# Optimization experiments

Measured on AMD Instinct MI355X. Metric: run time of the kernel, lower is better.

The kernel has to match this reference:

```python
import jax, jax.numpy as jnp
import numpy as np

N = 50000      # nodes
E = 1_600_000  # edges
F_IN = 128; HID = 128; LAT = 64; OUT = 128; GEN = 2


def gcn_conv(x, src, dst, norm, W, b, n_nodes):
    """PyG GCNConv with self-loops already appended to (src, dst) and
    symmetric normalization `norm` precomputed per edge."""
    h = x @ W                                    # [N, out]
    msg = h[src] * norm[:, None]                 # [E+N, out] gather + scale
    out = jax.ops.segment_sum(msg, dst, num_segments=n_nodes)
    return out + b


def _self_loop_norm(edge_index, n_nodes):
    loops = jnp.arange(n_nodes, dtype=edge_index.dtype)
    src = jnp.concatenate([edge_index[0], loops])
    dst = jnp.concatenate([edge_index[1], loops])
    deg = jnp.zeros((n_nodes,), jnp.float32).at[dst].add(1.0)
    dinv = jnp.where(deg > 0, deg ** -0.5, 0.0)
    norm = dinv[src] * dinv[dst]
    return src, dst, norm


def setup_inputs() -> dict:
    key = jax.random.key(0)
    ks = jax.random.split(key, 12)
    p = lambda k, s: jax.random.normal(k, s, jnp.float32) * 0.05
    return {
        "x": jax.random.normal(ks[0], (N, F_IN), jnp.float32),
        "edge_index": jax.random.randint(ks[1], (2, E), 0, N, jnp.int32),
        "eps": jax.random.normal(ks[2], (N, LAT), jnp.float32),
        "u": jax.random.uniform(ks[3], (N, GEN), jnp.float32),
        "W1": p(ks[4], (F_IN, HID)), "b1": jnp.zeros((HID,), jnp.float32),
        "W_mu": p(ks[5], (HID, LAT)), "b_mu": jnp.zeros((LAT,), jnp.float32),
        "W_ls": p(ks[6], (HID, LAT)), "b_ls": jnp.zeros((LAT,), jnp.float32),
        "W_dx": p(ks[7], (LAT, OUT)), "b_dx": jnp.zeros((OUT,), jnp.float32),
        "W_g": p(ks[8], (LAT, GEN)), "b_g": jnp.zeros((GEN,), jnp.float32),
        "W_lc": p(ks[9], (LAT, 1)), "b_lc": jnp.zeros((1,), jnp.float32),
    }


def reference(x, edge_index, eps, u, W1, b1, W_mu, b_mu, W_ls, b_ls,
              W_dx, b_dx, W_g, b_g, W_lc, b_lc):
    n = x.shape[0]
    src, dst, norm = _self_loop_norm(edge_index, n)

    # Encoder: GCN -> relu -> (mu, logvar)
    h = jax.nn.relu(gcn_conv(x, src, dst, norm, W1, b1, n))
    mu = gcn_conv(h, src, dst, norm, W_mu, b_mu, n)
    logvar = gcn_conv(h, src, dst, norm, W_ls, b_ls, n)

    # reparameterize: z = eps * exp(0.5*logvar) + mu
    z = eps * jnp.exp(0.5 * logvar) + mu

    # decoders / classifiers
    recon_x = gcn_conv(z, src, dst, norm, W_dx, b_dx, n)
    logits_gender = gcn_conv(z, src, dst, norm, W_g, b_g, n)
    logits_label = z @ W_lc + b_lc

    # Gumbel-softmax (hard, straight-through), temperature=1.0
    g = -jnp.log(-jnp.log(u + 1e-20) + 1e-20)
    y_soft = jax.nn.softmax(logits_gender + g, axis=-1)
    y_hard = jax.nn.one_hot(jnp.argmax(y_soft, axis=-1), GEN, dtype=y_soft.dtype)
    gender = jax.lax.stop_gradient(y_hard - y_soft) + y_soft

    return (recon_x, gender, logits_label, mu, logvar, z)
```

## Files before the change

### kernel.cpp

```cpp
#include <hip/hip_runtime.h>
#include <hip/hip_fp16.h>
#include <cstddef>


constexpr int R = 200;
constexpr int NBUCK = 250;
constexpr int NBLK = 250;
constexpr int SLABCAP = 12288;

__global__ __launch_bounds__(256) void hist_kernel(
    const int* __restrict__ dst, int* __restrict__ gh, int e, int chunk) {
  __shared__ int h[NBUCK];
  for (int t = threadIdx.x; t < NBUCK; t += 256) h[t] = 0;
  __syncthreads();
  int beg = blockIdx.x * chunk;
  int fin = min(e, beg + chunk);
  for (int i = beg + threadIdx.x; i < fin; i += 256)
    atomicAdd(&h[dst[i] / R], 1);
  __syncthreads();
  for (int t = threadIdx.x; t < NBUCK; t += 256)
    gh[t * NBLK + blockIdx.x] = h[t];
}

__global__ void scan_p1(const int* __restrict__ in, int* __restrict__ part, int n) {
  __shared__ int s[256];
  int i = blockIdx.x * 256 + threadIdx.x;
  s[threadIdx.x] = (i < n) ? in[i] : 0;
  __syncthreads();
  for (int off = 128; off > 0; off >>= 1) {
    if (threadIdx.x < off) s[threadIdx.x] += s[threadIdx.x + off];
    __syncthreads();
  }
  if (threadIdx.x == 0) part[blockIdx.x] = s[0];
}

__global__ void scan_p2(int* __restrict__ part, int nb, int* __restrict__ total_out) {
  __shared__ int s[256];
  int v = (threadIdx.x < nb) ? part[threadIdx.x] : 0;
  s[threadIdx.x] = v;
  __syncthreads();
  for (int off = 1; off < 256; off <<= 1) {
    int t = (threadIdx.x >= off) ? s[threadIdx.x - off] : 0;
    __syncthreads();
    s[threadIdx.x] += t;
    __syncthreads();
  }
  if (threadIdx.x < nb) part[threadIdx.x] = s[threadIdx.x] - v;
  if (threadIdx.x == nb - 1) *total_out = s[threadIdx.x];
}

__global__ void scan_p3(int* io, const int* __restrict__ part, int n) {
  __shared__ int s[256];
  int i = blockIdx.x * 256 + threadIdx.x;
  int v = (i < n) ? io[i] : 0;
  s[threadIdx.x] = v;
  __syncthreads();
  for (int off = 1; off < 256; off <<= 1) {
    int t = (threadIdx.x >= off) ? s[threadIdx.x - off] : 0;
    __syncthreads();
    s[threadIdx.x] += t;
    __syncthreads();
  }
  int excl = s[threadIdx.x] - v + part[blockIdx.x];
  if (i < n) io[i] = excl;
}

__global__ __launch_bounds__(256) void scatter_kernel(
    const int* __restrict__ src, const int* __restrict__ dst,
    const int* __restrict__ ghs, int* __restrict__ binned, int e, int chunk) {
  __shared__ int cur[NBUCK];
  for (int t = threadIdx.x; t < NBUCK; t += 256)
    cur[t] = ghs[t * NBLK + blockIdx.x];
  __syncthreads();
  int beg = blockIdx.x * chunk;
  int fin = min(e, beg + chunk);
  for (int i = beg + threadIdx.x; i < fin; i += 256) {
    int d = dst[i];
    int b = d / R;
    int p = atomicAdd(&cur[b], 1);
    binned[p] = ((d - b * R) << 16) | src[i];
  }
}

__global__ __launch_bounds__(256) void final_kernel(
    const int* __restrict__ binned, const int* __restrict__ ghs,
    int* __restrict__ rowptr, int* __restrict__ csr,
    float* __restrict__ dinv, int n, int e) {
  __shared__ int sdeg[R];
  __shared__ int sscan[256];
  __shared__ int scur[R];
  __shared__ int slab[SLABCAP];
  const int b = blockIdx.x;
  const int tid = threadIdx.x;
  const int base = ghs[b * NBLK];
  const int end = (b < NBUCK - 1) ? ghs[(b + 1) * NBLK] : e;
  const int cnt = end - base;

  if (tid < R) sdeg[tid] = 0;
  __syncthreads();
  for (int k = base + tid; k < end; k += 256)
    atomicAdd(&sdeg[binned[k] >> 16], 1);
  __syncthreads();

  int dv = (tid < R) ? sdeg[tid] : 0;
  sscan[tid] = dv;
  __syncthreads();
  for (int off = 1; off < 256; off <<= 1) {
    int t = (tid >= off) ? sscan[tid - off] : 0;
    __syncthreads();
    sscan[tid] += t;
    __syncthreads();
  }
  int excl = sscan[tid] - dv;
  int node = b * R + tid;
  if (tid < R && node < n) {
    rowptr[node] = base + excl;
    dinv[node] = 1.0f / sqrtf((float)dv + 1.0f);
    scur[tid] = excl;
  }
  __syncthreads();

  const bool fits = (cnt <= SLABCAP);
  for (int k = base + tid; k < end; k += 256) {
    int rec = binned[k];
    int p = atomicAdd(&scur[rec >> 16], 1);
    int s = rec & 0xFFFF;
    if (fits) slab[p] = s;
    else csr[base + p] = s;
  }
  __syncthreads();
  if (fits)
    for (int k = tid; k < cnt; k += 256) csr[base + k] = slab[k];
}

template <int K, int M, int KT, int RPT, bool BIAS, bool RELU, bool HALF_OUT>
__global__ __launch_bounds__(256, 4) void gemm_kernel(
    const float* __restrict__ A, const float* __restrict__ W,
    const float* __restrict__ bias, float* __restrict__ C,
    __half* __restrict__ Ch, const float* __restrict__ dinv, int n) {
  constexpr int CG = M / 4;
  constexpr int RS = 256 / CG;
  constexpr int RPB = RS * RPT;
  __shared__ float sW[KT * M];
  const int cg = threadIdx.x % CG;
  const int rs = threadIdx.x / CG;
  const int row0 = blockIdx.x * RPB + rs * RPT;

  const float* Arow[RPT];
#pragma unroll
  for (int rr = 0; rr < RPT; ++rr) {
    int row = row0 + rr;
    if (row > n - 1) row = n - 1;
    Arow[rr] = A + (size_t)row * K;
  }

  float4 acc[RPT];
#pragma unroll
  for (int rr = 0; rr < RPT; ++rr) acc[rr] = float4{0.f, 0.f, 0.f, 0.f};

  for (int kt = 0; kt < K; kt += KT) {
    if (kt) __syncthreads();
    for (int i = threadIdx.x * 4; i < KT * M; i += 1024)
      *reinterpret_cast<float4*>(&sW[i]) =
          *reinterpret_cast<const float4*>(&W[kt * M + i]);
    __syncthreads();
#pragma unroll 4
    for (int k4 = 0; k4 < KT; k4 += 4) {
      float4 a[RPT];
#pragma unroll
      for (int rr = 0; rr < RPT; ++rr)
        a[rr] = *reinterpret_cast<const float4*>(Arow[rr] + kt + k4);
#pragma unroll
      for (int j = 0; j < 4; ++j) {
        float4 w = *reinterpret_cast<const float4*>(&sW[(k4 + j) * M + cg * 4]);
#pragma unroll
        for (int rr = 0; rr < RPT; ++rr) {
          float av = reinterpret_cast<const float*>(&a[rr])[j];
          acc[rr].x += av * w.x;
          acc[rr].y += av * w.y;
          acc[rr].z += av * w.z;
          acc[rr].w += av * w.w;
        }
      }
    }
  }

  float4 bv = float4{0.f, 0.f, 0.f, 0.f};
  if (BIAS) bv = *reinterpret_cast<const float4*>(&bias[cg * 4]);
#pragma unroll
  for (int rr = 0; rr < RPT; ++rr) {
    int row = row0 + rr;
    if (row < n) {
      float4 o = acc[rr];
      if (BIAS) { o.x += bv.x; o.y += bv.y; o.z += bv.z; o.w += bv.w; }
      if (RELU) {
        o.x = fmaxf(o.x, 0.f); o.y = fmaxf(o.y, 0.f);
        o.z = fmaxf(o.z, 0.f); o.w = fmaxf(o.w, 0.f);
      }
      if (HALF_OUT) {
        float di = dinv[row];
        __half2* dst = reinterpret_cast<__half2*>(Ch + (size_t)row * M + cg * 4);
        dst[0] = __floats2half2_rn(di * o.x, di * o.y);
        dst[1] = __floats2half2_rn(di * o.z, di * o.w);
      } else {
        *reinterpret_cast<float4*>(&C[(size_t)row * M + cg * 4]) = o;
      }
    }
  }
}

template <int VAR, bool BIAS, bool RELU, bool HALF_OUT>
__global__ __launch_bounds__(256) void spmm128_kernel(
    const __half* __restrict__ Xs, void* __restrict__ Yout,
    const int* __restrict__ rowptr, const int* __restrict__ csr,
    const float* __restrict__ dinv, const float* __restrict__ bias, int n) {
  int wid = (blockIdx.x * blockDim.x + threadIdx.x) >> 6;
  int lane = threadIdx.x & 63;
  if (wid >= n) return;
  int beg = rowptr[wid];
  int end = rowptr[wid + 1];
  constexpr int U = (VAR == 0) ? 8 : 16;
  constexpr int NA = 8;
  float a0[NA], a1[NA];
#pragma unroll
  for (int uu = 0; uu < NA; ++uu) { a0[uu] = 0.f; a1[uu] = 0.f; }

  for (int base = beg; base < end; base += 64) {
    int m = end - base;
    if (m > 64) m = 64;
    int idx = (lane < m) ? csr[base + lane] : 0;
    int j = 0;
    for (; j + U <= m; j += U) {
      const __half2* rows[U];
#pragma unroll
      for (int uu = 0; uu < U; ++uu)
        rows[uu] = reinterpret_cast<const __half2*>(
            Xs + (size_t)__shfl(idx, j + uu, 64) * 128);
      __half2 v[U];
#pragma unroll
      for (int uu = 0; uu < U; ++uu) v[uu] = rows[uu][lane];
#pragma unroll
      for (int uu = 0; uu < U; ++uu) {
        float2 f = __half22float2(v[uu]);
        a0[uu & (NA - 1)] += f.x;
        a1[uu & (NA - 1)] += f.y;
      }
    }
    for (; j < m; ++j) {
      const __half2* row = reinterpret_cast<const __half2*>(
          Xs + (size_t)__shfl(idx, j, 64) * 128);
      float2 f = __half22float2(row[lane]);
      a0[0] += f.x;
      a1[0] += f.y;
    }
  }

  float t0 = 0.f, t1 = 0.f;
#pragma unroll
  for (int uu = 0; uu < NA; ++uu) { t0 += a0[uu]; t1 += a1[uu]; }

  float2 sf = __half22float2(
      reinterpret_cast<const __half2*>(Xs + (size_t)wid * 128)[lane]);
  t0 += sf.x;
  t1 += sf.y;

  float di = dinv[wid];
  float r0 = di * t0;
  float r1 = di * t1;
  if (BIAS) { r0 += bias[lane * 2]; r1 += bias[lane * 2 + 1]; }
  if (RELU) { r0 = fmaxf(r0, 0.f); r1 = fmaxf(r1, 0.f); }

  if (HALF_OUT) {
    reinterpret_cast<__half2*>((__half*)Yout + (size_t)wid * 128)[lane] =
        __floats2half2_rn(di * r0, di * r1);
  } else {
    float2 o = {r0, r1};
    reinterpret_cast<float2*>((float*)Yout + (size_t)wid * 128)[lane] = o;
  }
}

__global__ __launch_bounds__(256, 4) void mlz_kernel(
    const float* __restrict__ hagg,
    const float* __restrict__ Wmu, const float* __restrict__ bmu,
    const float* __restrict__ Wls, const float* __restrict__ bls,
    const float* __restrict__ eps, const float* __restrict__ dinv,
    const float* __restrict__ Wg, const float* __restrict__ Wlc,
    const float* __restrict__ blc,
    float* __restrict__ out_mu, float* __restrict__ out_lv,
    float* __restrict__ out_z, unsigned int* __restrict__ zh8,
    float2* __restrict__ zgs, float* __restrict__ out_label, int n) {
  constexpr int K = 128, M = 64, KT = 64, RPT = 4;
  constexpr int CG = M / 4;
  constexpr int RS = 256 / CG;
  constexpr int RPB = RS * RPT;
  __shared__ float sWm[KT * M];
  __shared__ float sWl[KT * M];
  const int cg = threadIdx.x % CG;
  const int rs = threadIdx.x / CG;
  const int row0 = blockIdx.x * RPB + rs * RPT;

  const float* Arow[RPT];
#pragma unroll
  for (int rr = 0; rr < RPT; ++rr) {
    int row = row0 + rr;
    if (row > n - 1) row = n - 1;
    Arow[rr] = hagg + (size_t)row * K;
  }

  float4 am[RPT], al[RPT];
#pragma unroll
  for (int rr = 0; rr < RPT; ++rr) {
    am[rr] = float4{0.f, 0.f, 0.f, 0.f};
    al[rr] = float4{0.f, 0.f, 0.f, 0.f};
  }

  for (int kt = 0; kt < K; kt += KT) {
    if (kt) __syncthreads();
    for (int i = threadIdx.x * 4; i < KT * M; i += 1024) {
      *reinterpret_cast<float4*>(&sWm[i]) =
          *reinterpret_cast<const float4*>(&Wmu[kt * M + i]);
      *reinterpret_cast<float4*>(&sWl[i]) =
          *reinterpret_cast<const float4*>(&Wls[kt * M + i]);
    }
    __syncthreads();
#pragma unroll 2
    for (int k4 = 0; k4 < KT; k4 += 4) {
      float4 a[RPT];
#pragma unroll
      for (int rr = 0; rr < RPT; ++rr)
        a[rr] = *reinterpret_cast<const float4*>(Arow[rr] + kt + k4);
#pragma unroll
      for (int j = 0; j < 4; ++j) {
        float4 wm = *reinterpret_cast<const float4*>(&sWm[(k4 + j) * M + cg * 4]);
        float4 wl = *reinterpret_cast<const float4*>(&sWl[(k4 + j) * M + cg * 4]);
#pragma unroll
        for (int rr = 0; rr < RPT; ++rr) {
          float av = reinterpret_cast<const float*>(&a[rr])[j];
          am[rr].x += av * wm.x; am[rr].y += av * wm.y;
          am[rr].z += av * wm.z; am[rr].w += av * wm.w;
          al[rr].x += av * wl.x; al[rr].y += av * wl.y;
          al[rr].z += av * wl.z; al[rr].w += av * wl.w;
        }
      }
    }
  }

  float4 bm = *reinterpret_cast<const float4*>(&bmu[cg * 4]);
  float4 bl = *reinterpret_cast<const float4*>(&bls[cg * 4]);
  float wg0[4], wg1[4], wlcv[4];
#pragma unroll
  for (int cc = 0; cc < 4; ++cc) {
    int c = cg * 4 + cc;
    wg0[cc] = Wg[c * 2 + 0];
    wg1[cc] = Wg[c * 2 + 1];
    wlcv[cc] = Wlc[c];
  }
  float blc0 = blc[0];

#pragma unroll
  for (int rr = 0; rr < RPT; ++rr) {
    int row = row0 + rr;
    if (row < n) {
      float4 mu4 = {am[rr].x + bm.x, am[rr].y + bm.y,
                    am[rr].z + bm.z, am[rr].w + bm.w};
      float4 lv4 = {al[rr].x + bl.x, al[rr].y + bl.y,
                    al[rr].z + bl.z, al[rr].w + bl.w};
      float4 e4 = *reinterpret_cast<const float4*>(&eps[(size_t)row * 64 + cg * 4]);
      float4 z4 = {e4.x * expf(0.5f * lv4.x) + mu4.x,
                   e4.y * expf(0.5f * lv4.y) + mu4.y,
                   e4.z * expf(0.5f * lv4.z) + mu4.z,
                   e4.w * expf(0.5f * lv4.w) + mu4.w};
      *reinterpret_cast<float4*>(&out_mu[(size_t)row * 64 + cg * 4]) = mu4;
      *reinterpret_cast<float4*>(&out_lv[(size_t)row * 64 + cg * 4]) = lv4;
      *reinterpret_cast<float4*>(&out_z[(size_t)row * 64 + cg * 4]) = z4;
      float di = dinv[row];
      int pw = __builtin_amdgcn_cvt_pk_fp8_f32(di * z4.x, di * z4.y, 0, false);
      pw = __builtin_amdgcn_cvt_pk_fp8_f32(di * z4.z, di * z4.w, pw, true);
      zh8[(size_t)row * 16 + cg] = (unsigned int)pw;
      float pg0 = z4.x * wg0[0] + z4.y * wg0[1] + z4.z * wg0[2] + z4.w * wg0[3];
      float pg1 = z4.x * wg1[0] + z4.y * wg1[1] + z4.z * wg1[2] + z4.w * wg1[3];
      float pl  = z4.x * wlcv[0] + z4.y * wlcv[1] + z4.z * wlcv[2] + z4.w * wlcv[3];
#pragma unroll
      for (int off = 1; off < 16; off <<= 1) {
        pg0 += __shfl_xor(pg0, off, 64);
        pg1 += __shfl_xor(pg1, off, 64);
        pl  += __shfl_xor(pl, off, 64);
      }
      if (cg == 0) {
        zgs[row] = float2{di * pg0, di * pg1};
        out_label[row] = pl + blc0;
      }
    }
  }
}

__device__ __forceinline__ void fp8x4acc(unsigned d, float* a) {
#if defined(__has_builtin) && __has_builtin(__builtin_amdgcn_cvt_pk_f32_fp8)
  typedef float f32x2 __attribute__((ext_vector_type(2)));
  f32x2 lo = __builtin_amdgcn_cvt_pk_f32_fp8((int)d, false);
  f32x2 hi = __builtin_amdgcn_cvt_pk_f32_fp8((int)d, true);
  a[0] += lo.x; a[1] += lo.y; a[2] += hi.x; a[3] += hi.y;
#else
  a[0] += __builtin_amdgcn_cvt_f32_fp8((int)d, 0);
  a[1] += __builtin_amdgcn_cvt_f32_fp8((int)d, 1);
  a[2] += __builtin_amdgcn_cvt_f32_fp8((int)d, 2);
  a[3] += __builtin_amdgcn_cvt_f32_fp8((int)d, 3);
#endif
}

__global__ __launch_bounds__(256) void spmm_zg_kernel(
    const unsigned char* __restrict__ zh8, const float2* __restrict__ zgs,
    float* __restrict__ zagg, const int* __restrict__ rowptr,
    const int* __restrict__ csr, const float* __restrict__ dinv,
    const float* __restrict__ bg, const float* __restrict__ u,
    float* __restrict__ out_gender, int n) {
  int wid = (blockIdx.x * blockDim.x + threadIdx.x) >> 6;
  int lane = threadIdx.x & 63;
  if (wid >= n) return;
  int beg = rowptr[wid];
  int end = rowptr[wid + 1];
  const int g = lane >> 4;
  const int c = lane & 15;
  const int coff = c * 4;

  float accA[4], accB[4];
#pragma unroll
  for (int f = 0; f < 4; ++f) { accA[f] = 0.f; accB[f] = 0.f; }
  float ga0 = 0.f, ga1 = 0.f;

  for (int base = beg; base < end; base += 64) {
    int m = end - base;
    if (m > 64) m = 64;
    int idx = 0;
    if (lane < m) {
      idx = csr[base + lane];
      float2 gz = zgs[idx];
      ga0 += gz.x;
      ga1 += gz.y;
    }
    int j = 0;
    for (; j + 8 <= m; j += 8) {
      int i0 = __shfl(idx, j + g, 64);
      int i1 = __shfl(idx, j + 4 + g, 64);
      unsigned d0 = *reinterpret_cast<const unsigned*>(
          zh8 + (size_t)(unsigned)i0 * 64 + coff);
      unsigned d1 = *reinterpret_cast<const unsigned*>(
          zh8 + (size_t)(unsigned)i1 * 64 + coff);
      fp8x4acc(d0, accA);
      fp8x4acc(d1, accB);
    }
    if (j < m) {
      int e0 = j + g;
      int e1 = j + 4 + g;
      int i0 = __shfl(idx, min(e0, m - 1), 64);
      int i1 = __shfl(idx, min(e1, m - 1), 64);
      unsigned d0 = *reinterpret_cast<const unsigned*>(
          zh8 + (size_t)(unsigned)i0 * 64 + coff);
      unsigned d1 = *reinterpret_cast<const unsigned*>(
          zh8 + (size_t)(unsigned)i1 * 64 + coff);
      if (e0 >= m) d0 = 0u;
      if (e1 >= m) d1 = 0u;
      fp8x4acc(d0, accA);
      fp8x4acc(d1, accB);
    }
  }

  float t[4];
#pragma unroll
  for (int f = 0; f < 4; ++f) t[f] = accA[f] + accB[f];
#pragma unroll
  for (int f = 0; f < 4; ++f) t[f] += __shfl_xor(t[f], 16, 64);
#pragma unroll
  for (int f = 0; f < 4; ++f) t[f] += __shfl_xor(t[f], 32, 64);

  float di = dinv[wid];
  if (lane < 16) {
    unsigned ds = *reinterpret_cast<const unsigned*>(
        zh8 + (size_t)wid * 64 + coff);
    fp8x4acc(ds, t);
    float4 o = {di * t[0], di * t[1], di * t[2], di * t[3]};
    *reinterpret_cast<float4*>(&zagg[(size_t)wid * 64 + 4 * c]) = o;
  }

  for (int off = 32; off > 0; off >>= 1) {
    ga0 += __shfl_xor(ga0, off, 64);
    ga1 += __shfl_xor(ga1, off, 64);
  }
  if (lane == 0) {
    float2 self = zgs[wid];
    ga0 += self.x;
    ga1 += self.y;
    float lg0 = di * ga0 + bg[0];
    float lg1 = di * ga1 + bg[1];
    float u0 = u[(size_t)wid * 2 + 0];
    float u1 = u[(size_t)wid * 2 + 1];
    float g0 = -logf(-logf(u0 + 1e-20f) + 1e-20f);
    float g1 = -logf(-logf(u1 + 1e-20f) + 1e-20f);
    float a0 = lg0 + g0, a1 = lg1 + g1;
    float mx = fmaxf(a0, a1);
    float e0 = expf(a0 - mx), e1 = expf(a1 - mx);
    float s = e0 + e1;
    float y0 = e0 / s, y1 = e1 / s;
    float h0 = (y1 > y0) ? 0.f : 1.f;
    float h1 = 1.f - h0;
    out_gender[(size_t)wid * 2 + 0] = (h0 - y0) + y0;
    out_gender[(size_t)wid * 2 + 1] = (h1 - y1) + y1;
  }
}

extern "C" void kernel_launch(void* const* d_in, const int* in_sizes, int n_in,
                              void* d_out, int out_size, void* d_ws, size_t ws_size,
                              hipStream_t stream) {
  const float* x   = (const float*)d_in[0];
  const int*   ei  = (const int*)d_in[1];
  const float* eps = (const float*)d_in[2];
  const float* u   = (const float*)d_in[3];
  const float* W1  = (const float*)d_in[4];
  const float* b1  = (const float*)d_in[5];
  const float* Wmu = (const float*)d_in[6];
  const float* bmu = (const float*)d_in[7];
  const float* Wls = (const float*)d_in[8];
  const float* bls = (const float*)d_in[9];
  const float* Wdx = (const float*)d_in[10];
  const float* bdx = (const float*)d_in[11];
  const float* Wg  = (const float*)d_in[12];
  const float* bg  = (const float*)d_in[13];
  const float* Wlc = (const float*)d_in[14];
  const float* blc = (const float*)d_in[15];

  const int n = in_sizes[0] / 128;
  const int e = in_sizes[1] / 2;
  const int* esrc = ei;
  const int* edst = ei + e;

  float* out = (float*)d_out;
  float* out_recon  = out;
  float* out_gender = out + (size_t)n * 128;
  float* out_label  = out_gender + (size_t)n * 2;
  float* out_mu     = out_label + n;
  float* out_lv     = out_mu + (size_t)n * 64;
  float* out_z      = out_lv + (size_t)n * 64;

  char* w = (char*)d_ws;
  size_t off = 0;
  auto alloc = [&](size_t bytes) {
    char* p = w + off;
    off = (off + bytes + 255) & ~(size_t)255;
    return p;
  };
  float* dinv  = (float*)alloc((size_t)n * 4);
  int* rowptr  = (int*)alloc((size_t)(n + 1) * 4);
  int* part    = (int*)alloc(256 * 4);
  int* csr     = (int*)alloc((size_t)e * 4);
  int* gh      = (int*)alloc((size_t)NBUCK * NBLK * 4);
  __half* Xs   = (__half*)alloc((size_t)n * 128 * 2);
  __half* hb   = (__half*)alloc((size_t)n * 128 * 2);
  float2* zgs  = (float2*)alloc((size_t)n * 8);
  unsigned char* zh8 = (unsigned char*)Xs;
  float* zagg  = (float*)hb;
  float* hagg  = out_recon;
  int* binned  = (int*)out_lv;

  const int GH = NBUCK * NBLK;
  const int GHB = (GH + 255) / 256;
  const int chunk = (e + NBLK - 1) / NBLK;

  hist_kernel<<<NBLK, 256, 0, stream>>>(edst, gh, e, chunk);
  scan_p1<<<GHB, 256, 0, stream>>>(gh, part, GH);
  scan_p2<<<1, 256, 0, stream>>>(part, GHB, &rowptr[n]);
  scan_p3<<<GHB, 256, 0, stream>>>(gh, part, GH);
  scatter_kernel<<<NBLK, 256, 0, stream>>>(esrc, edst, gh, binned, e, chunk);
  final_kernel<<<NBUCK, 256, 0, stream>>>(binned, gh, rowptr, csr, dinv, n, e);

  gemm_kernel<128, 128, 64, 4, false, false, true>
      <<<(n + 31) / 32, 256, 0, stream>>>(x, W1, nullptr, nullptr, Xs, dinv, n);
  spmm128_kernel<1, true, true, true>
      <<<(n + 3) / 4, 256, 0, stream>>>(Xs, hb, rowptr, csr, dinv, b1, n);
  spmm128_kernel<0, false, false, false>
      <<<(n + 3) / 4, 256, 0, stream>>>(hb, hagg, rowptr, csr, dinv, nullptr, n);
  mlz_kernel<<<(n + 63) / 64, 256, 0, stream>>>(
      hagg, Wmu, bmu, Wls, bls, eps, dinv, Wg, Wlc, blc,
      out_mu, out_lv, out_z, (unsigned int*)zh8, zgs, out_label, n);
  spmm_zg_kernel<<<(n + 3) / 4, 256, 0, stream>>>(
      zh8, (const float2*)zgs, zagg, rowptr, csr, dinv, bg, u, out_gender, n);
  gemm_kernel<64, 128, 64, 4, true, false, false>
      <<<(n + 31) / 32, 256, 0, stream>>>(zagg, Wdx, bdx, out_recon, nullptr, nullptr, n);
}
```

Measured before the change: 419.1 us.

## Fuse histogram with first GEMM, single-pass bucket scan, move dinv scaling into SpMM

The first feature GEMM no longer depends on dinv. It now runs in the same launch as the edge histogram, with extra blocks appended to the grid, so the two independent stages overlap. The source-side dinv scaling moves into the first SpMM as a per-neighbour gather of dinv. The three-kernel scan is replaced by one kernel that computes bucket totals and per-block offsets into a separate ghs buffer. This removes launches and serialisation but adds a scalar dinv load per neighbour in the first SpMM and lowers its unroll from 16 to 8.

```diff
diff --git a/kernel.cpp b/kernel.cpp
--- a/kernel.cpp
+++ b/kernel.cpp
@@ -8,61 +8,121 @@
 constexpr int NBLK = 250;
 constexpr int SLABCAP = 12288;
 
-__global__ __launch_bounds__(256) void hist_kernel(
-    const int* __restrict__ dst, int* __restrict__ gh, int e, int chunk) {
+__global__ __launch_bounds__(256, 4) void hist_gemm_kernel(
+    const int* __restrict__ dst, int* __restrict__ gh, int e, int chunk,
+    const float* __restrict__ A, const float* __restrict__ W,
+    __half* __restrict__ Ch, int n) {
+  constexpr int K = 128, M = 128, KT = 64, RPT = 4;
+  constexpr int CG = M / 4;
+  constexpr int RS = 256 / CG;
+  constexpr int RPB = RS * RPT;
+  __shared__ float sW[KT * M];
   __shared__ int h[NBUCK];
-  for (int t = threadIdx.x; t < NBUCK; t += 256) h[t] = 0;
-  __syncthreads();
-  int beg = blockIdx.x * chunk;
-  int fin = min(e, beg + chunk);
-  for (int i = beg + threadIdx.x; i < fin; i += 256)
-    atomicAdd(&h[dst[i] / R], 1);
-  __syncthreads();
-  for (int t = threadIdx.x; t < NBUCK; t += 256)
-    gh[t * NBLK + blockIdx.x] = h[t];
-}
-
-__global__ void scan_p1(const int* __restrict__ in, int* __restrict__ part, int n) {
+
+  if (blockIdx.x < (unsigned)NBLK) {
+    for (int t = threadIdx.x; t < NBUCK; t += 256) h[t] = 0;
+    __syncthreads();
+    int beg = blockIdx.x * chunk;
+    int fin = min(e, beg + chunk);
+    for (int i = beg + threadIdx.x; i < fin; i += 256)
+      atomicAdd(&h[dst[i] / R], 1);
+    __syncthreads();
+    for (int t = threadIdx.x; t < NBUCK; t += 256)
+      gh[t * NBLK + blockIdx.x] = h[t];
+    return;
+  }
+
+  const int bid = blockIdx.x - NBLK;
+  const int cg = threadIdx.x % CG;
+  const int rs = threadIdx.x / CG;
+  const int row0 = bid * RPB + rs * RPT;
+
+  const float* Arow[RPT];
+#pragma unroll
+  for (int rr = 0; rr < RPT; ++rr) {
+    int row = row0 + rr;
+    if (row > n - 1) row = n - 1;
+    Arow[rr] = A + (size_t)row * K;
+  }
+
+  float4 acc[RPT];
+#pragma unroll
+  for (int rr = 0; rr < RPT; ++rr) acc[rr] = float4{0.f, 0.f, 0.f, 0.f};
+
+  for (int kt = 0; kt < K; kt += KT) {
+    if (kt) __syncthreads();
+    for (int i = threadIdx.x * 4; i < KT * M; i += 1024)
+      *reinterpret_cast<float4*>(&sW[i]) =
+          *reinterpret_cast<const float4*>(&W[kt * M + i]);
+    __syncthreads();
+#pragma unroll 4
+    for (int k4 = 0; k4 < KT; k4 += 4) {
+      float4 a[RPT];
+#pragma unroll
+      for (int rr = 0; rr < RPT; ++rr)
+        a[rr] = *reinterpret_cast<const float4*>(Arow[rr] + kt + k4);
+#pragma unroll
+      for (int j = 0; j < 4; ++j) {
+        float4 w = *reinterpret_cast<const float4*>(&sW[(k4 + j) * M + cg * 4]);
+#pragma unroll
+        for (int rr = 0; rr < RPT; ++rr) {
+          float av = reinterpret_cast<const float*>(&a[rr])[j];
+          acc[rr].x += av * w.x;
+          acc[rr].y += av * w.y;
+          acc[rr].z += av * w.z;
+          acc[rr].w += av * w.w;
+        }
+      }
+    }
+  }
+
+#pragma unroll
+  for (int rr = 0; rr < RPT; ++rr) {
+    int row = row0 + rr;
+    if (row < n) {
+      __half2* d2 = reinterpret_cast<__half2*>(Ch + (size_t)row * M + cg * 4);
+      d2[0] = __floats2half2_rn(acc[rr].x, acc[rr].y);
+      d2[1] = __floats2half2_rn(acc[rr].z, acc[rr].w);
+    }
+  }
+}
+
+__global__ __launch_bounds__(256) void bscan_kernel(
+    const int* __restrict__ gh, int* __restrict__ ghs,
+    int* __restrict__ rowptr_n) {
   __shared__ int s[256];
-  int i = blockIdx.x * 256 + threadIdx.x;
-  s[threadIdx.x] = (i < n) ? in[i] : 0;
-  __syncthreads();
-  for (int off = 128; off > 0; off >>= 1) {
-    if (threadIdx.x < off) s[threadIdx.x] += s[threadIdx.x + off];
-    __syncthreads();
-  }
-  if (threadIdx.x == 0) part[blockIdx.x] = s[0];
-}
-
-__global__ void scan_p2(int* __restrict__ part, int nb, int* __restrict__ total_out) {
-  __shared__ int s[256];
-  int v = (threadIdx.x < nb) ? part[threadIdx.x] : 0;
-  s[threadIdx.x] = v;
+  __shared__ int sBase[NBUCK + 1];
+  const int b = blockIdx.x;
+  const int tid = threadIdx.x;
+
+  int tot = 0;
+  if (tid < NBUCK) {
+    const int* row = gh + tid * NBLK;
+    for (int k = 0; k < NBLK; ++k) tot += row[k];
+  }
+  s[tid] = tot;
   __syncthreads();
   for (int off = 1; off < 256; off <<= 1) {
-    int t = (threadIdx.x >= off) ? s[threadIdx.x - off] : 0;
-    __syncthreads();
-    s[threadIdx.x] += t;
-    __syncthreads();
-  }
-  if (threadIdx.x < nb) part[threadIdx.x] = s[threadIdx.x] - v;
-  if (threadIdx.x == nb - 1) *total_out = s[threadIdx.x];
-}
-
-__global__ void scan_p3(int* io, const int* __restrict__ part, int n) {
-  __shared__ int s[256];
-  int i = blockIdx.x * 256 + threadIdx.x;
-  int v = (i < n) ? io[i] : 0;
-  s[threadIdx.x] = v;
+    int t = (tid >= off) ? s[tid - off] : 0;
+    __syncthreads();
+    s[tid] += t;
+    __syncthreads();
+  }
+  if (tid < NBUCK) sBase[tid] = s[tid] - tot;
+  if (tid == NBUCK - 1) sBase[NBUCK] = s[tid];
+  __syncthreads();
+
+  int v = (tid < NBLK) ? gh[b * NBLK + tid] : 0;
+  s[tid] = v;
   __syncthreads();
   for (int off = 1; off < 256; off <<= 1) {
-    int t = (threadIdx.x >= off) ? s[threadIdx.x - off] : 0;
-    __syncthreads();
-    s[threadIdx.x] += t;
-    __syncthreads();
-  }
-  int excl = s[threadIdx.x] - v + part[blockIdx.x];
-  if (i < n) io[i] = excl;
+    int t = (tid >= off) ? s[tid - off] : 0;
+    __syncthreads();
+    s[tid] += t;
+    __syncthreads();
+  }
+  if (tid < NBLK) ghs[b * NBLK + tid] = s[tid] - v + sBase[b];
+  if (b == 0 && tid == 0) *rowptr_n = sBase[NBUCK];
 }
 
 __global__ __launch_bounds__(256) void scatter_kernel(
@@ -133,11 +193,10 @@
     for (int k = tid; k < cnt; k += 256) csr[base + k] = slab[k];
 }
 
-template <int K, int M, int KT, int RPT, bool BIAS, bool RELU, bool HALF_OUT>
+template <int K, int M, int KT, int RPT, bool BIAS>
 __global__ __launch_bounds__(256, 4) void gemm_kernel(
     const float* __restrict__ A, const float* __restrict__ W,
-    const float* __restrict__ bias, float* __restrict__ C,
-    __half* __restrict__ Ch, const float* __restrict__ dinv, int n) {
+    const float* __restrict__ bias, float* __restrict__ C, int n) {
   constexpr int CG = M / 4;
   constexpr int RS = 256 / CG;
   constexpr int RPB = RS * RPT;
@@ -193,23 +252,12 @@
     if (row < n) {
       float4 o = acc[rr];
       if (BIAS) { o.x += bv.x; o.y += bv.y; o.z += bv.z; o.w += bv.w; }
-      if (RELU) {
-        o.x = fmaxf(o.x, 0.f); o.y = fmaxf(o.y, 0.f);
-        o.z = fmaxf(o.z, 0.f); o.w = fmaxf(o.w, 0.f);
-      }
-      if (HALF_OUT) {
-        float di = dinv[row];
-        __half2* dst = reinterpret_cast<__half2*>(Ch + (size_t)row * M + cg * 4);
-        dst[0] = __floats2half2_rn(di * o.x, di * o.y);
-        dst[1] = __floats2half2_rn(di * o.z, di * o.w);
-      } else {
-        *reinterpret_cast<float4*>(&C[(size_t)row * M + cg * 4]) = o;
-      }
-    }
-  }
-}
-
-template <int VAR, bool BIAS, bool RELU, bool HALF_OUT>
+      *reinterpret_cast<float4*>(&C[(size_t)row * M + cg * 4]) = o;
+    }
+  }
+}
+
+template <bool SRCSCALE, bool BIAS, bool RELU, bool HALF_OUT>
 __global__ __launch_bounds__(256) void spmm128_kernel(
     const __half* __restrict__ Xs, void* __restrict__ Yout,
     const int* __restrict__ rowptr, const int* __restrict__ csr,
@@ -219,11 +267,10 @@
   if (wid >= n) return;
   int beg = rowptr[wid];
   int end = rowptr[wid + 1];
-  constexpr int U = (VAR == 0) ? 8 : 16;
-  constexpr int NA = 8;
-  float a0[NA], a1[NA];
-#pragma unroll
-  for (int uu = 0; uu < NA; ++uu) { a0[uu] = 0.f; a1[uu] = 0.f; }
+  constexpr int U = 8;
+  float a0[U], a1[U];
+#pragma unroll
+  for (int uu = 0; uu < U; ++uu) { a0[uu] = 0.f; a1[uu] = 0.f; }
 
   for (int base = beg; base < end; base += 64) {
     int m = end - base;
@@ -232,39 +279,59 @@
     int j = 0;
     for (; j + U <= m; j += U) {
       const __half2* rows[U];
-#pragma unroll
-      for (int uu = 0; uu < U; ++uu)
-        rows[uu] = reinterpret_cast<const __half2*>(
-            Xs + (size_t)__shfl(idx, j + uu, 64) * 128);
+      float ds[U];
+#pragma unroll
+      for (int uu = 0; uu < U; ++uu) {
+        int i = __shfl(idx, j + uu, 64);
+        rows[uu] = reinterpret_cast<const __half2*>(Xs + (size_t)i * 128);
+        if (SRCSCALE) ds[uu] = dinv[i];
+      }
       __half2 v[U];
 #pragma unroll
       for (int uu = 0; uu < U; ++uu) v[uu] = rows[uu][lane];
 #pragma unroll
       for (int uu = 0; uu < U; ++uu) {
         float2 f = __half22float2(v[uu]);
-        a0[uu & (NA - 1)] += f.x;
-        a1[uu & (NA - 1)] += f.y;
+        if (SRCSCALE) {
+          a0[uu] += ds[uu] * f.x;
+          a1[uu] += ds[uu] * f.y;
+        } else {
+          a0[uu] += f.x;
+          a1[uu] += f.y;
+        }
       }
     }
     for (; j < m; ++j) {
-      const __half2* row = reinterpret_cast<const __half2*>(
-          Xs + (size_t)__shfl(idx, j, 64) * 128);
+      int i = __shfl(idx, j, 64);
+      const __half2* row = reinterpret_cast<const __half2*>(Xs + (size_t)i * 128);
       float2 f = __half22float2(row[lane]);
-      a0[0] += f.x;
-      a1[0] += f.y;
+      if (SRCSCALE) {
+        float ds = dinv[i];
+        a0[0] += ds * f.x;
+        a1[0] += ds * f.y;
+      } else {
+        a0[0] += f.x;
+        a1[0] += f.y;
+      }
     }
   }
 
   float t0 = 0.f, t1 = 0.f;
 #pragma unroll
-  for (int uu = 0; uu < NA; ++uu) { t0 += a0[uu]; t1 += a1[uu]; }
+  for (int uu = 0; uu < U; ++uu) { t0 += a0[uu]; t1 += a1[uu]; }
+
+  float di = dinv[wid];
 
   float2 sf = __half22float2(
       reinterpret_cast<const __half2*>(Xs + (size_t)wid * 128)[lane]);
-  t0 += sf.x;
-  t1 += sf.y;
-
-  float di = dinv[wid];
+  if (SRCSCALE) {
+    t0 += di * sf.x;
+    t1 += di * sf.y;
+  } else {
+    t0 += sf.x;
+    t1 += sf.y;
+  }
+
   float r0 = di * t0;
   float r1 = di * t1;
   if (BIAS) { r0 += bias[lane * 2]; r1 += bias[lane * 2 + 1]; }
@@ -550,9 +617,9 @@
   };
   float* dinv  = (float*)alloc((size_t)n * 4);
   int* rowptr  = (int*)alloc((size_t)(n + 1) * 4);
-  int* part    = (int*)alloc(256 * 4);
   int* csr     = (int*)alloc((size_t)e * 4);
   int* gh      = (int*)alloc((size_t)NBUCK * NBLK * 4);
+  int* ghs     = (int*)alloc((size_t)NBUCK * NBLK * 4);
   __half* Xs   = (__half*)alloc((size_t)n * 128 * 2);
   __half* hb   = (__half*)alloc((size_t)n * 128 * 2);
   float2* zgs  = (float2*)alloc((size_t)n * 8);
@@ -561,28 +628,24 @@
   float* hagg  = out_recon;
   int* binned  = (int*)out_lv;
 
-  const int GH = NBUCK * NBLK;
-  const int GHB = (GH + 255) / 256;
   const int chunk = (e + NBLK - 1) / NBLK;
-
-  hist_kernel<<<NBLK, 256, 0, stream>>>(edst, gh, e, chunk);
-  scan_p1<<<GHB, 256, 0, stream>>>(gh, part, GH);
-  scan_p2<<<1, 256, 0, stream>>>(part, GHB, &rowptr[n]);
-  scan_p3<<<GHB, 256, 0, stream>>>(gh, part, GH);
-  scatter_kernel<<<NBLK, 256, 0, stream>>>(esrc, edst, gh, binned, e, chunk);
-  final_kernel<<<NBUCK, 256, 0, stream>>>(binned, gh, rowptr, csr, dinv, n, e);
-
-  gemm_kernel<128, 128, 64, 4, false, false, true>
-      <<<(n + 31) / 32, 256, 0, stream>>>(x, W1, nullptr, nullptr, Xs, dinv, n);
-  spmm128_kernel<1, true, true, true>
+  const int GBLK = (n + 31) / 32;
+
+  hist_gemm_kernel<<<NBLK + GBLK, 256, 0, stream>>>(
+      edst, gh, e, chunk, x, W1, Xs, n);
+  bscan_kernel<<<NBUCK, 256, 0, stream>>>(gh, ghs, &rowptr[n]);
+  scatter_kernel<<<NBLK, 256, 0, stream>>>(esrc, edst, ghs, binned, e, chunk);
+  final_kernel<<<NBUCK, 256, 0, stream>>>(binned, ghs, rowptr, csr, dinv, n, e);
+
+  spmm128_kernel<true, true, true, true>
       <<<(n + 3) / 4, 256, 0, stream>>>(Xs, hb, rowptr, csr, dinv, b1, n);
-  spmm128_kernel<0, false, false, false>
+  spmm128_kernel<false, false, false, false>
       <<<(n + 3) / 4, 256, 0, stream>>>(hb, hagg, rowptr, csr, dinv, nullptr, n);
   mlz_kernel<<<(n + 63) / 64, 256, 0, stream>>>(
       hagg, Wmu, bmu, Wls, bls, eps, dinv, Wg, Wlc, blc,
       out_mu, out_lv, out_z, (unsigned int*)zh8, zgs, out_label, n);
   spmm_zg_kernel<<<(n + 3) / 4, 256, 0, stream>>>(
       zh8, (const float2*)zgs, zagg, rowptr, csr, dinv, bg, u, out_gender, n);
-  gemm_kernel<64, 128, 64, 4, true, false, false>
-      <<<(n + 31) / 32, 256, 0, stream>>>(zagg, Wdx, bdx, out_recon, nullptr, nullptr, n);
-}
+  gemm_kernel<64, 128, 64, 4, true>
+      <<<GBLK, 256, 0, stream>>>(zagg, Wdx, bdx, out_recon, n);
+}
```

New measurement: 411.1 us. About the same (-1.9%).
